# Optimization experiments

Measured on AMD Instinct MI355X. Metric: run time of the kernel, lower is better.

The kernel has to match this reference:

```python
import jax, jax.numpy as jnp
import numpy as np


def _species_mlp(x, W1, b1, W2, b2, W3, b3, W4, b4):
    # x: [S, A, F] per-species feature blocks; weights: [S, ...] per-species MLPs
    h = jax.nn.silu(jnp.einsum('saf,sfh->sah', x, W1) + b1[:, None, :])
    h = jax.nn.silu(jnp.einsum('sah,shk->sak', h, W2) + b2[:, None, :])
    h = jax.nn.silu(jnp.einsum('sak,skm->sam', h, W3) + b3[:, None, :])
    e = jnp.einsum('sam,smo->sao', h, W4) + b4[:, None, :]  # [S, A, 1]
    return e[..., 0]  # atomic energies [S, A]


def setup_inputs() -> dict:
    key = jax.random.key(0)
    ks = jax.random.split(key, 12)
    S, A, F, H = 4, 32768, 512, 256
    n_structures = 512
    w = 0.05  # keep activations in a sane range
    return {
        'features': jax.random.normal(ks[0], (S, A, F), dtype=jnp.float32),
        'struct_ids': jax.random.randint(ks[1], (S, A), 0, n_structures),
        'W1': jax.random.normal(ks[2], (S, F, H), dtype=jnp.float32) * w,
        'b1': jax.random.normal(ks[3], (S, H), dtype=jnp.float32) * w,
        'W2': jax.random.normal(ks[4], (S, H, H), dtype=jnp.float32) * w,
        'b2': jax.random.normal(ks[5], (S, H), dtype=jnp.float32) * w,
        'W3': jax.random.normal(ks[6], (S, H, H), dtype=jnp.float32) * w,
        'b3': jax.random.normal(ks[7], (S, H), dtype=jnp.float32) * w,
        'W4': jax.random.normal(ks[8], (S, H, 1), dtype=jnp.float32) * w,
        'b4': jax.random.normal(ks[9], (S, 1), dtype=jnp.float32) * w,
        'energy_shift': jax.random.normal(ks[10], (1,), dtype=jnp.float32),
        'n_structures': n_structures,
    }


def reference(features, struct_ids, W1, b1, W2, b2, W3, b3, W4, b4, energy_shift, n_structures):
    # per-species MLP over all blocks (the per-species gather is the block layout itself)
    atomic_energies = _species_mlp(features, W1, b1, W2, b2, W3, b3, W4, b4)  # [S, A]
    # index_add scatter of atomic energies into per-structure energies
    energies = jax.ops.segment_sum(
        atomic_energies.reshape(-1), struct_ids.reshape(-1), num_segments=n_structures
    )
    energies = energies + energy_shift[0]
    return energies
```

## Files before the change

kernel.cpp:

```cpp
#include <hip/hip_runtime.h>

typedef _Float16 f16x8 __attribute__((ext_vector_type(8)));
typedef _Float16 f16x4 __attribute__((ext_vector_type(4)));
typedef float f32x4 __attribute__((ext_vector_type(4)));

static constexpr int S = 4;
static constexpr int NATOMS = 32768;
static constexpr int FIN = 512;
static constexpr int H = 256;
static constexpr int BM = 64;
static constexpr int XSTR = 72;
static constexpr int HSTR = 264;

__global__ void pack_w(const float* __restrict__ W, _Float16* __restrict__ dst, int KT, int l1) {
    int idx = blockIdx.x * 256 + threadIdx.x;
    int j = idx & 7;
    int lane = (idx >> 3) & 63;
    int rest = idx >> 9;
    int kt = rest % KT;
    int t2 = rest / KT;
    int K = KT * 32;
    int k = kt * 32 + (lane >> 4) * 8 + j;
    int ntile = t2 & 15;
    int s = t2 >> 4;
    int n = ntile * 16 + (lane & 15);
    int p = l1 ? ((kt >> 1) * 4 + (kt & 1) * 2 + (ntile & 1))
               : (kt * 2 + (ntile & 1));
    size_t o = ((((size_t)(s * 8 + (ntile >> 1))) * (KT * 2) + p) * 64 + lane) * 8 + j;
    dst[o] = (_Float16)W[((size_t)s * K + k) * H + n];
}

__global__ void init_out(float* __restrict__ out, const float* __restrict__ shift, int n) {
    int i = blockIdx.x * 256 + threadIdx.x;
    if (i < n) out[i] = shift[0];
}

__global__ __launch_bounds__(512, 4) void fused_mlp(
    const float* __restrict__ X, const int* __restrict__ ids,
    const _Float16* __restrict__ W1p, const _Float16* __restrict__ W2p,
    const _Float16* __restrict__ W3p,
    const float* __restrict__ b1, const float* __restrict__ b2,
    const float* __restrict__ b3,
    const float* __restrict__ W4, const float* __restrict__ b4,
    float* __restrict__ out)
{
    __shared__ _Float16 smem[BM * HSTR];
    __shared__ float e_lds[8][BM];

    const int s = blockIdx.y;
    const int tile = blockIdx.x;
    const int tid = threadIdx.x;
    const int rw = __builtin_amdgcn_readfirstlane(tid >> 6);
    const int lane = tid & 63;
    const int g = lane >> 4;
    const int mh = lane & 15;
    const int srow = tid >> 3;
    const int cq = tid & 7;

    const float* Xb = X + (size_t)(s * NATOMS + tile * BM) * FIN;
    _Float16* hb = smem;

    const _Float16* Wb1 = W1p + ((size_t)(s * 8 + rw)) * (32 * 512) + lane * 8;
    const _Float16* Wb2 = W2p + ((size_t)(s * 8 + rw)) * (16 * 512) + lane * 8;
    const _Float16* Wb3 = W3p + ((size_t)(s * 8 + rw)) * (16 * 512) + lane * 8;

    f32x4 acc[4][2];
#pragma unroll
    for (int i = 0; i < 4; ++i)
#pragma unroll
        for (int j = 0; j < 2; ++j)
            acc[i][j] = f32x4{0.f, 0.f, 0.f, 0.f};

    f32x4 ld[4][2];
    auto loadc = [&](int slot, int c) {
        const float* p = Xb + (size_t)srow * FIN + c * 64 + cq * 8;
        ld[slot][0] = *(const f32x4*)(p);
        ld[slot][1] = *(const f32x4*)(p + 4);
    };
    auto storec = [&](int slot, int c) {
        _Float16* xb = smem + (c % 3) * (BM * XSTR);
#pragma unroll
        for (int i = 0; i < 2; ++i) {
            f16x4 v;
#pragma unroll
            for (int j = 0; j < 4; ++j) v[j] = (_Float16)ld[slot][i][j];
            *(f16x4*)(xb + srow * XSTR + cq * 8 + i * 4) = v;
        }
    };
    auto l1mfma = [&](int c) {
        const _Float16* xb = smem + (c % 3) * (BM * XSTR);
#pragma unroll
        for (int ks = 0; ks < 2; ++ks) {
            f16x8 a[4];
#pragma unroll
            for (int mt = 0; mt < 4; ++mt)
                a[mt] = *(const f16x8*)(xb + (mt * 16 + mh) * XSTR + (ks * 4 + g) * 8);
            __builtin_amdgcn_s_setprio(1);
#pragma unroll
            for (int nt = 0; nt < 2; ++nt) {
                f16x8 b = *(const f16x8*)(Wb1 + (c * 4 + ks * 2 + nt) * 512);
#pragma unroll
                for (int mt = 0; mt < 4; ++mt)
                    acc[mt][nt] = __builtin_amdgcn_mfma_f32_16x16x32_f16(a[mt], b, acc[mt][nt], 0, 0, 0);
            }
            __builtin_amdgcn_s_setprio(0);
        }
    };

    loadc(0, 0);
    loadc(1, 1);
    loadc(2, 2);
    loadc(3, 3);
    storec(0, 0);
    asm volatile("s_waitcnt lgkmcnt(0)" ::: "memory");
    __builtin_amdgcn_s_barrier();
#pragma unroll
    for (int c = 0; c < 8; ++c) {
        if (c < 7) storec((c + 1) & 3, c + 1);
        if (c < 4) loadc(c & 3, c + 4);
        l1mfma(c);
        asm volatile("s_waitcnt lgkmcnt(0)" ::: "memory");
        __builtin_amdgcn_s_barrier();
    }
    __syncthreads();

    {
        float bv[2];
#pragma unroll
        for (int nt = 0; nt < 2; ++nt) bv[nt] = b1[s * H + rw * 32 + nt * 16 + mh];
#pragma unroll
        for (int mt = 0; mt < 4; ++mt)
#pragma unroll
            for (int nt = 0; nt < 2; ++nt)
#pragma unroll
                for (int r = 0; r < 4; ++r) {
                    float v = acc[mt][nt][r] + bv[nt];
                    v = __fdividef(v, 1.f + __expf(-v));
                    hb[(mt * 16 + g * 4 + r) * HSTR + rw * 32 + nt * 16 + mh] = (_Float16)v;
                    acc[mt][nt][r] = 0.f;
                }
    }
    __syncthreads();

    for (int l = 0; l < 2; ++l) {
        const _Float16* Wb = l ? Wb3 : Wb2;
#pragma unroll
        for (int ks = 0; ks < 8; ++ks) {
            f16x8 a[4];
#pragma unroll
            for (int mt = 0; mt < 4; ++mt)
                a[mt] = *(const f16x8*)(hb + (mt * 16 + mh) * HSTR + ks * 32 + g * 8);
            __builtin_amdgcn_s_setprio(1);
#pragma unroll
            for (int nt = 0; nt < 2; ++nt) {
                f16x8 b = *(const f16x8*)(Wb + (ks * 2 + nt) * 512);
#pragma unroll
                for (int mt = 0; mt < 4; ++mt)
                    acc[mt][nt] = __builtin_amdgcn_mfma_f32_16x16x32_f16(a[mt], b, acc[mt][nt], 0, 0, 0);
            }
            __builtin_amdgcn_s_setprio(0);
        }
        __syncthreads();
        if (l == 0) {
            float bv[2];
#pragma unroll
            for (int nt = 0; nt < 2; ++nt) bv[nt] = b2[s * H + rw * 32 + nt * 16 + mh];
#pragma unroll
            for (int mt = 0; mt < 4; ++mt)
#pragma unroll
                for (int nt = 0; nt < 2; ++nt)
#pragma unroll
                    for (int r = 0; r < 4; ++r) {
                        float v = acc[mt][nt][r] + bv[nt];
                        v = __fdividef(v, 1.f + __expf(-v));
                        hb[(mt * 16 + g * 4 + r) * HSTR + rw * 32 + nt * 16 + mh] = (_Float16)v;
                        acc[mt][nt][r] = 0.f;
                    }
            __syncthreads();
        }
    }

    {
        float bv[2], w4v[2];
#pragma unroll
        for (int nt = 0; nt < 2; ++nt) {
            int col = rw * 32 + nt * 16 + mh;
            bv[nt] = b3[s * H + col];
            w4v[nt] = W4[s * H + col];
        }
#pragma unroll
        for (int mt = 0; mt < 4; ++mt)
#pragma unroll
            for (int r = 0; r < 4; ++r) {
                float v = 0.f;
#pragma unroll
                for (int nt = 0; nt < 2; ++nt) {
                    float h = acc[mt][nt][r] + bv[nt];
                    h = __fdividef(h, 1.f + __expf(-h));
                    v += h * w4v[nt];
                }
                v += __shfl_xor(v, 1);
                v += __shfl_xor(v, 2);
                v += __shfl_xor(v, 4);
                v += __shfl_xor(v, 8);
                if (mh == r) e_lds[rw][mt * 16 + g * 4 + r] = v;
            }
    }
    __syncthreads();
    if (tid < BM) {
        float e = b4[s];
#pragma unroll
        for (int j = 0; j < 8; ++j) e += e_lds[j][tid];
        int id = ids[s * NATOMS + tile * BM + tid];
        atomicAdd(&out[id], e);
    }
}

extern "C" void kernel_launch(void* const* d_in, const int* in_sizes, int n_in,
                              void* d_out, int out_size, void* d_ws, size_t ws_size,
                              hipStream_t stream) {
    const float* X   = (const float*)d_in[0];
    const int*   ids = (const int*)d_in[1];
    const float* W1  = (const float*)d_in[2];
    const float* b1  = (const float*)d_in[3];
    const float* W2  = (const float*)d_in[4];
    const float* b2  = (const float*)d_in[5];
    const float* W3  = (const float*)d_in[6];
    const float* b3  = (const float*)d_in[7];
    const float* W4  = (const float*)d_in[8];
    const float* b4  = (const float*)d_in[9];
    const float* shift = (const float*)d_in[10];

    _Float16* W1p = (_Float16*)d_ws;
    _Float16* W2p = W1p + (size_t)S * 8 * 32 * 512;
    _Float16* W3p = W2p + (size_t)S * 8 * 16 * 512;

    pack_w<<<2048, 256, 0, stream>>>(W1, W1p, 16, 1);
    pack_w<<<1024, 256, 0, stream>>>(W2, W2p, 8, 0);
    pack_w<<<1024, 256, 0, stream>>>(W3, W3p, 8, 0);

    init_out<<<(out_size + 255) / 256, 256, 0, stream>>>((float*)d_out, shift, out_size);

    dim3 grid(NATOMS / BM, S);
    fused_mlp<<<grid, 512, 0, stream>>>(X, ids, W1p, W2p, W3p, b1, b2, b3, W4, b4,
                                        (float*)d_out);
}
```

Before: 162.2 us.

## Replace global atomic scatter with two-stage LDS-histogram segment reduction

Rather than each tile issuing global atomicAdds into the 512 structure energies, the MLP kernel now writes per-atom energies to a workspace buffer. A reduce kernel then builds per-block histograms with LDS atomics, and a second single-block kernel sums the 128 partial tables and adds the energy shift. This removes contended global atomics on a small output and the init kernel, and makes the result deterministic. In exchange it adds two launches plus extra global traffic for the per-atom energies and the partials.

```diff
diff --git a/kernel.cpp b/kernel.cpp
--- a/kernel.cpp
+++ b/kernel.cpp
@@ -11,6 +11,9 @@
 static constexpr int BM = 64;
 static constexpr int XSTR = 72;
 static constexpr int HSTR = 264;
+static constexpr int NSTRUCT = 512;
+static constexpr int RBLK = 128;
+static constexpr int APB = (S * NATOMS) / RBLK;
 
 __global__ void pack_w(const float* __restrict__ W, _Float16* __restrict__ dst, int KT, int l1) {
     int idx = blockIdx.x * 256 + threadIdx.x;
@@ -30,19 +33,14 @@
     dst[o] = (_Float16)W[((size_t)s * K + k) * H + n];
 }
 
-__global__ void init_out(float* __restrict__ out, const float* __restrict__ shift, int n) {
-    int i = blockIdx.x * 256 + threadIdx.x;
-    if (i < n) out[i] = shift[0];
-}
-
 __global__ __launch_bounds__(512, 4) void fused_mlp(
-    const float* __restrict__ X, const int* __restrict__ ids,
+    const float* __restrict__ X,
     const _Float16* __restrict__ W1p, const _Float16* __restrict__ W2p,
     const _Float16* __restrict__ W3p,
     const float* __restrict__ b1, const float* __restrict__ b2,
     const float* __restrict__ b3,
     const float* __restrict__ W4, const float* __restrict__ b4,
-    float* __restrict__ out)
+    float* __restrict__ Eout)
 {
     __shared__ _Float16 smem[BM * HSTR];
     __shared__ float e_lds[8][BM];
@@ -211,9 +209,40 @@
         float e = b4[s];
 #pragma unroll
         for (int j = 0; j < 8; ++j) e += e_lds[j][tid];
-        int id = ids[s * NATOMS + tile * BM + tid];
-        atomicAdd(&out[id], e);
-    }
+        Eout[(size_t)s * NATOMS + tile * BM + tid] = e;
+    }
+}
+
+__global__ __launch_bounds__(256) void reduce1(
+    const float* __restrict__ E, const int* __restrict__ ids,
+    float* __restrict__ partials)
+{
+    __shared__ float tbl[NSTRUCT];
+    const int b = blockIdx.x;
+    const int tid = threadIdx.x;
+    tbl[tid] = 0.f;
+    tbl[tid + 256] = 0.f;
+    __syncthreads();
+    const int base = b * APB;
+#pragma unroll
+    for (int i = 0; i < APB / 256; ++i) {
+        int a = base + i * 256 + tid;
+        atomicAdd(&tbl[ids[a]], E[a]);
+    }
+    __syncthreads();
+    partials[(size_t)b * NSTRUCT + tid] = tbl[tid];
+    partials[(size_t)b * NSTRUCT + tid + 256] = tbl[tid + 256];
+}
+
+__global__ __launch_bounds__(512) void reduce2(
+    const float* __restrict__ partials, const float* __restrict__ shift,
+    float* __restrict__ out)
+{
+    const int i = threadIdx.x;
+    float v = shift[0];
+#pragma unroll 8
+    for (int b = 0; b < RBLK; ++b) v += partials[(size_t)b * NSTRUCT + i];
+    out[i] = v;
 }
 
 extern "C" void kernel_launch(void* const* d_in, const int* in_sizes, int n_in,
@@ -234,14 +263,16 @@
     _Float16* W1p = (_Float16*)d_ws;
     _Float16* W2p = W1p + (size_t)S * 8 * 32 * 512;
     _Float16* W3p = W2p + (size_t)S * 8 * 16 * 512;
+    float* E = (float*)(W3p + (size_t)S * 8 * 16 * 512);
+    float* partials = E + (size_t)S * NATOMS;
 
     pack_w<<<2048, 256, 0, stream>>>(W1, W1p, 16, 1);
     pack_w<<<1024, 256, 0, stream>>>(W2, W2p, 8, 0);
     pack_w<<<1024, 256, 0, stream>>>(W3, W3p, 8, 0);
 
-    init_out<<<(out_size + 255) / 256, 256, 0, stream>>>((float*)d_out, shift, out_size);
-
     dim3 grid(NATOMS / BM, S);
-    fused_mlp<<<grid, 512, 0, stream>>>(X, ids, W1p, W2p, W3p, b1, b2, b3, W4, b4,
-                                        (float*)d_out);
-}
+    fused_mlp<<<grid, 512, 0, stream>>>(X, W1p, W2p, W3p, b1, b2, b3, W4, b4, E);
+
+    reduce1<<<RBLK, 256, 0, stream>>>(E, ids, partials);
+    reduce2<<<1, 512, 0, stream>>>(partials, shift, (float*)d_out);
+}
```

Measured after the change: 149.7 us. 7.7% less time.
